# Kernel optimization log

Hardware: AMD Instinct MI355X
Metric: run time of the kernel (lower is better)

## Reference

```python
import jax, jax.numpy as jnp
import numpy as np

COUNTS = [1536, 8192, 16384, 24576, 12288, 1024, 512, 512, 256, 128, 128]
OFFS = np.concatenate([[0], np.cumsum(COUNTS)]).astype(int).tolist()
N = OFFS[-1]          # 65536 atoms total, sorted by degree
MAX_DEG = 10
BATCH = 2048          # fixed GraphGather batch size
F_IN = 75
GC = 256
DENSE = 512
N_TASKS = 12
N_CLASSES = 2
BN_EPS = 1e-3         # keras BatchNormalization default epsilon


def _graph_conv(x, deg_adjs, w0, wself, wneigh, b):
    # deepchem GraphConv: per-degree (self @ Wself + sum_neighbors @ Wneigh + b), relu
    outs = [x[OFFS[0]:OFFS[1]] @ w0 + b[0]]  # degree-0 atoms: self transform only
    for d in range(1, MAX_DEG + 1):
        self_atoms = x[OFFS[d]:OFFS[d + 1]]            # [n_d, F]
        neigh = x[deg_adjs[d - 1]].sum(axis=1)         # gather [n_d, d, F] -> sum -> [n_d, F]
        outs.append(self_atoms @ wself[d - 1] + neigh @ wneigh[d - 1] + b[d])
    return jax.nn.relu(jnp.concatenate(outs, axis=0))


def _graph_pool(x, deg_adjs):
    # deepchem GraphPool: elementwise max over {self} U neighbors, per degree
    outs = [x[OFFS[0]:OFFS[1]]]  # degree-0 atoms pass through
    for d in range(1, MAX_DEG + 1):
        self_atoms = x[OFFS[d]:OFFS[d + 1]]
        outs.append(jnp.maximum(self_atoms, x[deg_adjs[d - 1]].max(axis=1)))
    return jnp.concatenate(outs, axis=0)


def _bn(x, g, bta, m, v):
    # inference-mode BatchNormalization (training=False -> moving stats)
    return g * (x - m) * jax.lax.rsqrt(v + BN_EPS) + bta


def setup_inputs():
    key = jax.random.key(0)
    ks = iter(jax.random.split(key, 64))
    inp = {}
    inp["atom_features"] = jax.random.normal(next(ks), (N, F_IN), jnp.float32)
    inp["degree_slice"] = jnp.asarray(
        np.stack([np.array(OFFS[:-1]), np.array(COUNTS)], axis=1), jnp.int32)
    # each molecule gets exactly N/BATCH atoms so no GraphGather segment is empty
    inp["membership"] = jax.random.permutation(
        next(ks), jnp.arange(N, dtype=jnp.int32) % BATCH)
    inp["n_samples"] = BATCH
    for d in range(1, MAX_DEG + 1):
        inp["deg_adj_%d" % d] = jax.random.randint(
            next(ks), (COUNTS[d], d), 0, N, jnp.int32)

    def lin(k, fi, fo):
        return jax.random.normal(k, (fi, fo), jnp.float32) * np.float32(1.0 / np.sqrt(fi))

    for li, fi in [(1, F_IN), (2, GC)]:
        inp["gc%d_w0" % li] = lin(next(ks), fi, GC)
        inp["gc%d_wself" % li] = jnp.stack([lin(next(ks), fi, GC) for _ in range(MAX_DEG)])
        inp["gc%d_wneigh" % li] = jnp.stack([lin(next(ks), fi, GC) for _ in range(MAX_DEG)])
        inp["gc%d_b" % li] = jnp.zeros((MAX_DEG + 1, GC), jnp.float32)
    for bi, dim in [(1, GC), (2, GC), (3, DENSE)]:
        inp["bn%d_gamma" % bi] = jnp.ones((dim,), jnp.float32)
        inp["bn%d_beta" % bi] = jnp.zeros((dim,), jnp.float32)
        inp["bn%d_mean" % bi] = jnp.zeros((dim,), jnp.float32)
        inp["bn%d_var" % bi] = jnp.ones((dim,), jnp.float32)
    inp["dense_w"] = lin(next(ks), GC, DENSE)
    inp["dense_b"] = jnp.zeros((DENSE,), jnp.float32)
    inp["out_w"] = lin(next(ks), 2 * DENSE, N_TASKS * N_CLASSES)
    inp["out_b"] = jnp.zeros((N_TASKS * N_CLASSES,), jnp.float32)
    return inp


def reference(atom_features, degree_slice, membership, n_samples,
              deg_adj_1, deg_adj_2, deg_adj_3, deg_adj_4, deg_adj_5,
              deg_adj_6, deg_adj_7, deg_adj_8, deg_adj_9, deg_adj_10,
              gc1_w0, gc1_wself, gc1_wneigh, gc1_b,
              gc2_w0, gc2_wself, gc2_wneigh, gc2_b,
              bn1_gamma, bn1_beta, bn1_mean, bn1_var,
              bn2_gamma, bn2_beta, bn2_mean, bn2_var,
              bn3_gamma, bn3_beta, bn3_mean, bn3_var,
              dense_w, dense_b, out_w, out_b):
    deg_adjs = [deg_adj_1, deg_adj_2, deg_adj_3, deg_adj_4, deg_adj_5,
                deg_adj_6, deg_adj_7, deg_adj_8, deg_adj_9, deg_adj_10]
    h = _graph_conv(atom_features, deg_adjs, gc1_w0, gc1_wself, gc1_wneigh, gc1_b)
    h = _bn(h, bn1_gamma, bn1_beta, bn1_mean, bn1_var)
    h = _graph_pool(h, deg_adjs)
    h = _graph_conv(h, deg_adjs, gc2_w0, gc2_wself, gc2_wneigh, gc2_b)
    h = _bn(h, bn2_gamma, bn2_beta, bn2_mean, bn2_var)
    h = _graph_pool(h, deg_adjs)
    h = jax.nn.relu(h @ dense_w + dense_b)
    h = _bn(h, bn3_gamma, bn3_beta, bn3_mean, bn3_var)
    # GraphGather: tanh(concat(segment_sum, segment_max))
    ssum = jax.ops.segment_sum(h, membership, num_segments=BATCH)
    smax = jax.ops.segment_max(h, membership, num_segments=BATCH)
    fp = jnp.tanh(jnp.concatenate([ssum, smax], axis=1))   # [BATCH, 2*DENSE]
    logits = (fp @ out_w + out_b).reshape(BATCH, N_TASKS, N_CLASSES)[:n_samples]
    probs = jax.nn.softmax(logits, axis=-1)
    return probs, logits, fp
```

## Files before the change

### kernel.cpp

```cpp
#include <hip/hip_runtime.h>
#include <hip/hip_fp16.h>
#include <math.h>

#define NATOMS 65536

typedef _Float16 f16_t;
typedef __attribute__((ext_vector_type(8))) _Float16 half8;
typedef __attribute__((ext_vector_type(4))) float f32x4;

__constant__ int c_offs[12] = {0,1536,9728,26112,50688,62976,64000,64512,65024,65280,65408,65536};

struct Adj { const int* p[10]; };

__device__ __forceinline__ int seg_of(int row) {
    int s = 0;
#pragma unroll
    for (int i = 1; i <= 10; ++i) s += (row >= c_offs[i]) ? 1 : 0;
    return s;
}

__device__ __forceinline__ void glds16(const f16_t* g, f16_t* l) {
    __builtin_amdgcn_global_load_lds(
        (const __attribute__((address_space(1))) unsigned int*)g,
        (__attribute__((address_space(3))) unsigned int*)l,
        16, 0, 0);
}


__global__ void pack_w1(const float* __restrict__ w0, const float* __restrict__ wself,
                        const float* __restrict__ wneigh, f16_t* __restrict__ Wp) {
    int idx = blockIdx.x * 256 + threadIdx.x;
    int j = idx & 7, lane = (idx >> 3) & 63;
    int kb = (idx >> 9) % 6;
    int rest = idx / (512 * 6);
    int ni = rest & 15, s = rest >> 4;
    int k = kb * 32 + (lane >> 4) * 8 + j;
    int n = ni * 16 + (lane & 15);
    float v = 0.f;
    if (k < 75) v = (s == 0) ? w0[k*256 + n] : wself[((s-1)*75 + k)*256 + n];
    else if (k >= 96 && k < 171 && s > 0) v = wneigh[((s-1)*75 + (k-96))*256 + n];
    Wp[idx] = (f16_t)v;
}

__global__ void pack_w2(const float* __restrict__ w0, const float* __restrict__ wself,
                        const float* __restrict__ wneigh, f16_t* __restrict__ Wp) {
    int idx = blockIdx.x * 256 + threadIdx.x;
    int j = idx & 7, lane = (idx >> 3) & 63;
    int kb = (idx >> 9) & 15;
    int rest = idx >> 13;
    int ni = rest & 15, s = rest >> 4;
    int k = kb * 32 + (lane >> 4) * 8 + j;
    int n = ni * 16 + (lane & 15);
    float v = 0.f;
    if (k < 256) v = (s == 0) ? w0[k*256 + n] : wself[((s-1)*256 + k)*256 + n];
    else if (s > 0) v = wneigh[((s-1)*256 + (k-256))*256 + n];
    Wp[idx] = (f16_t)v;
}

__global__ void pack_wd(const float* __restrict__ w, f16_t* __restrict__ Wp) {
    int idx = blockIdx.x * 256 + threadIdx.x;
    int j = idx & 7, lane = (idx >> 3) & 63;
    int kb = (idx >> 9) & 7;
    int ni = (idx >> 12) & 31;
    int k = kb * 32 + (lane >> 4) * 8 + j;
    int n = ni * 16 + (lane & 15);
    Wp[idx] = (f16_t)w[(size_t)k*512 + n];
}

__global__ void cvt_pad(const float* __restrict__ xf, f16_t* __restrict__ xq) {
    int idx = blockIdx.x * 256 + threadIdx.x;
    int r = idx / 96;
    int c = idx - r * 96;
    xq[idx] = (c < 75) ? (f16_t)xf[(size_t)r*75 + c] : (f16_t)0.f;
}

template<int D, bool ISMAX, int LD>
__device__ __forceinline__ void gathD(float* v, const f16_t* __restrict__ src,
                                      const int* __restrict__ ap, int c) {
    int rows[D];
#pragma unroll
    for (int j = 0; j < D; ++j) rows[j] = ap[j];
    uint4 raw[D];
#pragma unroll
    for (int j = 0; j < D; ++j) raw[j] = *(const uint4*)(src + (size_t)rows[j]*LD + c);
#pragma unroll
    for (int j = 0; j < D; ++j) {
        const f16_t* u = (const f16_t*)&raw[j];
#pragma unroll
        for (int e = 0; e < 8; ++e) {
            float f = (float)u[e];
            v[e] = ISMAX ? fmaxf(v[e], f) : (v[e] + f);
        }
    }
}

template<bool ISMAX, int LD>
__device__ __forceinline__ void gath_switch(float* v, const f16_t* __restrict__ src,
                                            const int* __restrict__ ap, int s, int c) {
    switch (s) {
        case 1:  gathD<1,ISMAX,LD>(v,src,ap,c);  break;
        case 2:  gathD<2,ISMAX,LD>(v,src,ap,c);  break;
        case 3:  gathD<3,ISMAX,LD>(v,src,ap,c);  break;
        case 4:  gathD<4,ISMAX,LD>(v,src,ap,c);  break;
        case 5:  gathD<5,ISMAX,LD>(v,src,ap,c);  break;
        case 6:  gathD<6,ISMAX,LD>(v,src,ap,c);  break;
        case 7:  gathD<7,ISMAX,LD>(v,src,ap,c);  break;
        case 8:  gathD<8,ISMAX,LD>(v,src,ap,c);  break;
        case 9:  gathD<9,ISMAX,LD>(v,src,ap,c);  break;
        case 10: gathD<10,ISMAX,LD>(v,src,ap,c); break;
        default: break;
    }
}

__global__ __launch_bounds__(256) void nbsum_x(const f16_t* __restrict__ xq, f16_t* __restrict__ NBX, Adj adj) {
    int idx = blockIdx.x * 256 + threadIdx.x;
    int r = idx >> 4;
    int cc = idx & 15;
    if (cc >= 12) return;
    int c = cc << 3;
    int s = seg_of(r);
    float v[8];
#pragma unroll
    for (int e = 0; e < 8; ++e) v[e] = 0.f;
    if (s > 0)
        gath_switch<false,96>(v, xq, adj.p[s-1] + (size_t)(r - c_offs[s]) * s, s, c);
    f16_t o[8];
#pragma unroll
    for (int e = 0; e < 8; ++e) o[e] = (f16_t)v[e];
    *(uint4*)(NBX + (size_t)r*96 + c) = *(uint4*)o;
}

__global__ __launch_bounds__(256) void pool_k(const f16_t* __restrict__ H, f16_t* __restrict__ P, Adj adj) {
    int idx = blockIdx.x * 256 + threadIdx.x;
    int r = idx >> 5;
    int c = (idx & 31) << 3;
    int s = seg_of(r);
    uint4 self = *(const uint4*)(H + (size_t)r*256 + c);
    const f16_t* hp = (const f16_t*)&self;
    float v[8];
#pragma unroll
    for (int e = 0; e < 8; ++e) v[e] = (float)hp[e];
    if (s > 0)
        gath_switch<true,256>(v, H, adj.p[s-1] + (size_t)(r - c_offs[s]) * s, s, c);
    f16_t o[8];
#pragma unroll
    for (int e = 0; e < 8; ++e) o[e] = (f16_t)v[e];
    *(uint4*)(P + (size_t)r*256 + c) = *(uint4*)o;
}

__global__ __launch_bounds__(256) void nbsum_k(const f16_t* __restrict__ P, f16_t* __restrict__ NB, Adj adj) {
    int idx = blockIdx.x * 256 + threadIdx.x;
    int r = idx >> 5;
    int c = (idx & 31) << 3;
    int s = seg_of(r);
    float v[8];
#pragma unroll
    for (int e = 0; e < 8; ++e) v[e] = 0.f;
    if (s > 0)
        gath_switch<false,256>(v, P, adj.p[s-1] + (size_t)(r - c_offs[s]) * s, s, c);
    f16_t o[8];
#pragma unroll
    for (int e = 0; e < 8; ++e) o[e] = (f16_t)v[e];
    *(uint4*)(NB + (size_t)r*256 + c) = *(uint4*)o;
}

template<int K, int KSPLIT, int LDA, int N, int NY, bool SEG>
__global__ __launch_bounds__(256)
void gemm_mfma(const f16_t* __restrict__ A0, const f16_t* __restrict__ A1,
               const f16_t* __restrict__ Wp,
               const float* __restrict__ bias,
               const float* __restrict__ bng, const float* __restrict__ bnb,
               const float* __restrict__ bnm, const float* __restrict__ bnv,
               f16_t* __restrict__ C)
{
    constexpr int NKB = K / 32;
    constexpr int NNT = N / 16;
    __shared__ char smem[17408];
    f16_t* sA = (f16_t*)smem;
    f16_t* sB = sA + 4096;
    f16_t* eps = (f16_t*)smem;

    const int t = threadIdx.x;
    const int lane = t & 63, wave = t >> 6;
    const int wm = wave >> 1, wn = wave & 1;
    const int quad = lane >> 4, l16 = lane & 15;
    const int id = blockIdx.x;
    const int xcd = id & 7;
    const int jj = id >> 3;
    const int xi = jj / NY;
    const int y  = jj - xi * NY;
    const int r0 = (xi * 8 + xcd) * 128;
    const int n0 = y * 128;
    const int seg = SEG ? seg_of(r0) : 0;
    const int nbase = n0 >> 4;

    f32x4 acc[4][4];
#pragma unroll
    for (int mi = 0; mi < 4; ++mi)
#pragma unroll
        for (int ni = 0; ni < 4; ++ni) acc[mi][ni] = (f32x4){0.f,0.f,0.f,0.f};

    size_t aoff[2];
#pragma unroll
    for (int i = 0; i < 2; ++i)
        aoff[i] = (size_t)(r0 + (wave*2 + i)*16 + l16) * LDA + quad*8;
    size_t bbase[2];
#pragma unroll
    for (int i = 0; i < 2; ++i)
        bbase[i] = ((size_t)(seg*NNT + nbase + wave*2 + i) * NKB) * 512 + lane*8;

#pragma unroll
    for (int kb = 0; kb < NKB; ++kb) {
        const int kg = kb * 32;
        const f16_t* Ab = (kg < KSPLIT) ? (A0 + kg) : (A1 + (kg - KSPLIT));
#pragma unroll
        for (int i = 0; i < 2; ++i) {
            glds16(Ab + aoff[i], sA + (wave*2 + i)*512);
            glds16(Wp + bbase[i] + (size_t)kb*512, sB + (wave*2 + i)*512);
        }
        __syncthreads();
        half8 a[4], b[4];
#pragma unroll
        for (int mi = 0; mi < 4; ++mi)
            a[mi] = *(const half8*)(sA + (wm*4 + mi)*512 + lane*8);
#pragma unroll
        for (int ni = 0; ni < 4; ++ni)
            b[ni] = *(const half8*)(sB + (wn*4 + ni)*512 + lane*8);
#pragma unroll
        for (int mi = 0; mi < 4; ++mi)
#pragma unroll
            for (int ni = 0; ni < 4; ++ni)
                acc[mi][ni] = __builtin_amdgcn_mfma_f32_16x16x32_f16(a[mi], b[ni], acc[mi][ni], 0, 0, 0);
        __syncthreads();
    }

#pragma unroll
    for (int p = 0; p < 2; ++p) {
        if (wm == p) {
#pragma unroll
            for (int ni = 0; ni < 4; ++ni) {
                const int lcol = (wn*4 + ni)*16 + l16;
                const int col = n0 + lcol;
                const float scale = bng[col] * rsqrtf(bnv[col] + 1e-3f);
                const float shift = bnb[col] - bnm[col] * scale;
                const float bv = bias[(SEG ? seg*N : 0) + col];
#pragma unroll
                for (int mi = 0; mi < 4; ++mi) {
                    const int lrowb = mi*16 + quad*4;
#pragma unroll
                    for (int r = 0; r < 4; ++r) {
                        float v = acc[mi][ni][r] + bv;
                        v = fmaxf(v, 0.f);
                        v = fmaf(v, scale, shift);
                        eps[(lrowb + r)*136 + lcol] = (f16_t)v;
                    }
                }
            }
        }
        __syncthreads();
#pragma unroll
        for (int it = 0; it < 4; ++it) {
            int row = it*16 + (t >> 4);
            int ch  = t & 15;
            uint4 v = *(const uint4*)&eps[row*136 + ch*8];
            *(uint4*)(C + (size_t)(r0 + p*64 + row)*N + n0 + ch*8) = v;
        }
        __syncthreads();
    }
}

__global__ void scatter_k(const int* __restrict__ mem, int* __restrict__ counts, int* __restrict__ slots) {
    int i = blockIdx.x * 256 + threadIdx.x;
    int s = mem[i];
    int p = atomicAdd(&counts[s], 1);
    if (p < 32) slots[s*32 + p] = i;
}

__global__ __launch_bounds__(256)
void reduce_k(const f16_t* __restrict__ H3, const int* __restrict__ slots, float* __restrict__ fp) {
    int s = blockIdx.x, t = threadIdx.x;
    const int* sl = slots + s*32;
    float s0 = 0.f, s1 = 0.f, m0 = -INFINITY, m1 = -INFINITY;
#pragma unroll
    for (int i = 0; i < 32; i += 4) {
        int a[4];
#pragma unroll
        for (int j = 0; j < 4; ++j) a[j] = sl[i+j];
        float v0[4], v1[4];
#pragma unroll
        for (int j = 0; j < 4; ++j) {
            const f16_t* hr = H3 + (size_t)a[j]*512;
            v0[j] = (float)hr[t]; v1[j] = (float)hr[t+256];
        }
#pragma unroll
        for (int j = 0; j < 4; ++j) {
            s0 += v0[j]; s1 += v1[j];
            m0 = fmaxf(m0, v0[j]); m1 = fmaxf(m1, v1[j]);
        }
    }
    float* fr = fp + (size_t)s*1024;
    fr[t]       = tanhf(s0);
    fr[t+256]   = tanhf(s1);
    fr[512+t]   = tanhf(m0);
    fr[768+t]   = tanhf(m1);
}

__global__ __launch_bounds__(256)
void final_k(const float* __restrict__ fp, const float* __restrict__ out_w,
             const float* __restrict__ out_b, float* __restrict__ probs, float* __restrict__ logits) {
    __shared__ float row[1024];
    __shared__ float lg[24];
    int s = blockIdx.x, t = threadIdx.x;
    const float* fr = fp + (size_t)s*1024;
    *(float4*)&row[t*4] = *(const float4*)&fr[t*4];
    __syncthreads();
    if (t < 192) {
        int o = t >> 3;
        int k0 = (t & 7) * 128;
        float acc = 0.f;
        for (int k = 0; k < 128; ++k)
            acc = fmaf(row[k0+k], out_w[(size_t)(k0+k)*24 + o], acc);
        acc += __shfl_xor(acc, 1);
        acc += __shfl_xor(acc, 2);
        acc += __shfl_xor(acc, 4);
        if ((t & 7) == 0) lg[o] = acc + out_b[o];
    }
    __syncthreads();
    if (t < 12) {
        float l0 = lg[2*t], l1 = lg[2*t+1];
        float m = fmaxf(l0, l1);
        float e0 = expf(l0-m), e1 = expf(l1-m);
        float inv = 1.f / (e0 + e1);
        int base = s*24 + 2*t;
        probs[base]   = e0*inv;  probs[base+1]  = e1*inv;
        logits[base]  = l0;      logits[base+1] = l1;
    }
}

extern "C" void kernel_launch(void* const* d_in, const int* in_sizes, int n_in,
                              void* d_out, int out_size, void* d_ws, size_t ws_size,
                              hipStream_t stream) {
    const float* atom       = (const float*)d_in[0];
    const int*   membership = (const int*)  d_in[2];
    Adj adj;
    for (int d = 0; d < 10; ++d) adj.p[d] = (const int*)d_in[4+d];
    const float* gc1_w0     = (const float*)d_in[14];
    const float* gc1_wself  = (const float*)d_in[15];
    const float* gc1_wneigh = (const float*)d_in[16];
    const float* gc1_b      = (const float*)d_in[17];
    const float* gc2_w0     = (const float*)d_in[18];
    const float* gc2_wself  = (const float*)d_in[19];
    const float* gc2_wneigh = (const float*)d_in[20];
    const float* gc2_b      = (const float*)d_in[21];
    const float* bn1g = (const float*)d_in[22]; const float* bn1b = (const float*)d_in[23];
    const float* bn1m = (const float*)d_in[24]; const float* bn1v = (const float*)d_in[25];
    const float* bn2g = (const float*)d_in[26]; const float* bn2b = (const float*)d_in[27];
    const float* bn2m = (const float*)d_in[28]; const float* bn2v = (const float*)d_in[29];
    const float* bn3g = (const float*)d_in[30]; const float* bn3b = (const float*)d_in[31];
    const float* bn3m = (const float*)d_in[32]; const float* bn3v = (const float*)d_in[33];
    const float* dense_w = (const float*)d_in[34];
    const float* dense_b = (const float*)d_in[35];
    const float* out_w   = (const float*)d_in[36];
    const float* out_b   = (const float*)d_in[37];

    f16_t* wsb = (f16_t*)d_ws;
    f16_t* xq   = wsb;
    f16_t* NBX  = wsb + 6291456;
    f16_t* H1b  = wsb + 12582912;
    f16_t* P1b  = wsb + 29360128;
    f16_t* NB2b = wsb + 46137344;
    f16_t* H2b  = H1b;
    f16_t* P2b  = NB2b;
    f16_t* H3b  = H1b;
    f16_t* W1p  = wsb + 62914560;
    f16_t* W2p  = wsb + 63455232;
    f16_t* Wdp  = wsb + 64897024;
    int*  counts = (int*)(wsb + 65028096);
    int*  slots  = counts + 2048;

    float* outp   = (float*)d_out;
    float* probs  = outp;
    float* logits = outp + 49152;
    float* fp     = outp + 98304;

    pack_w1<<<2112, 256, 0, stream>>>(gc1_w0, gc1_wself, gc1_wneigh, W1p);
    pack_w2<<<5632, 256, 0, stream>>>(gc2_w0, gc2_wself, gc2_wneigh, W2p);
    pack_wd<<<512,  256, 0, stream>>>(dense_w, Wdp);

    cvt_pad<<<(NATOMS*96)/256, 256, 0, stream>>>(atom, xq);
    nbsum_x<<<(NATOMS*16)/256, 256, 0, stream>>>(xq, NBX, adj);
    gemm_mfma<192,96,96,256,2,true><<<1024, 256, 0, stream>>>(
        xq, NBX, W1p, gc1_b, bn1g, bn1b, bn1m, bn1v, H1b);
    pool_k<<<(NATOMS*32)/256, 256, 0, stream>>>(H1b, P1b, adj);

    nbsum_k<<<(NATOMS*32)/256, 256, 0, stream>>>(P1b, NB2b, adj);
    gemm_mfma<512,256,256,256,2,true><<<1024, 256, 0, stream>>>(
        P1b, NB2b, W2p, gc2_b, bn2g, bn2b, bn2m, bn2v, H2b);
    pool_k<<<(NATOMS*32)/256, 256, 0, stream>>>(H2b, P2b, adj);

    gemm_mfma<256,256,256,512,4,false><<<2048, 256, 0, stream>>>(
        P2b, P2b, Wdp, dense_b, bn3g, bn3b, bn3m, bn3v, H3b);

    hipMemsetAsync((void*)counts, 0, 2048*sizeof(int), stream);
    scatter_k<<<NATOMS/256, 256, 0, stream>>>(membership, counts, slots);
    reduce_k<<<2048, 256, 0, stream>>>(H3b, slots, fp);

    final_k<<<2048, 256, 0, stream>>>(fp, out_w, out_b, probs, logits);
}
```

Baseline: 391.0 us.

## Compute output logits with MFMA GEMM and vectorize GraphGather reduction

The per-sample scalar output layer (one block per sample, with strided fp32 weight reads) is replaced by a batched f16 MFMA GEMM over all 2048 fingerprints against a packed, zero-padded output weight. Softmax is fused into the GEMM epilogue using a lane shuffle. The segment reduction now uses 64-thread blocks with 16-byte vector loads, and also writes an f16 copy of the fingerprint to feed the GEMM. This adds a weight-pack kernel, and the logits are computed from f16-rounded fingerprints, which lowers their precision.

```diff
diff --git a/kernel.cpp b/kernel.cpp
--- a/kernel.cpp
+++ b/kernel.cpp
@@ -65,6 +65,16 @@
     int k = kb * 32 + (lane >> 4) * 8 + j;
     int n = ni * 16 + (lane & 15);
     Wp[idx] = (f16_t)w[(size_t)k*512 + n];
+}
+
+__global__ void pack_wo(const float* __restrict__ w, f16_t* __restrict__ Wp) {
+    int idx = blockIdx.x * 256 + threadIdx.x;
+    int j = idx & 7, lane = (idx >> 3) & 63;
+    int kb = (idx >> 9) & 31;
+    int ni = idx >> 14;
+    int k = kb * 32 + (lane >> 4) * 8 + j;
+    int n = ni * 16 + (lane & 15);
+    Wp[idx] = (n < 24) ? (f16_t)w[k*24 + n] : (f16_t)0.f;
 }
 
 __global__ void cvt_pad(const float* __restrict__ xf, f16_t* __restrict__ xq) {
@@ -276,64 +286,116 @@
     if (p < 32) slots[s*32 + p] = i;
 }
 
+__global__ __launch_bounds__(64)
+void reduce_k(const f16_t* __restrict__ H3, const int* __restrict__ slots,
+              float* __restrict__ fp, f16_t* __restrict__ fph) {
+    int s = blockIdx.x, l = threadIdx.x;
+    int c = l * 8;
+    const int* sl = slots + s*32;
+    float sm[8], mx[8];
+#pragma unroll
+    for (int e = 0; e < 8; ++e) { sm[e] = 0.f; mx[e] = -INFINITY; }
+#pragma unroll
+    for (int i = 0; i < 32; ++i) {
+        int a = sl[i];
+        uint4 raw = *(const uint4*)(H3 + (size_t)a*512 + c);
+        const f16_t* u = (const f16_t*)&raw;
+#pragma unroll
+        for (int e = 0; e < 8; ++e) {
+            float f = (float)u[e];
+            sm[e] += f;
+            mx[e] = fmaxf(mx[e], f);
+        }
+    }
+    float o1[8], o2[8];
+    f16_t h1[8], h2[8];
+#pragma unroll
+    for (int e = 0; e < 8; ++e) {
+        o1[e] = tanhf(sm[e]); o2[e] = tanhf(mx[e]);
+        h1[e] = (f16_t)o1[e]; h2[e] = (f16_t)o2[e];
+    }
+    float* fr = fp + (size_t)s*1024;
+    *(float4*)(fr + c)       = *(float4*)&o1[0];
+    *(float4*)(fr + c + 4)   = *(float4*)&o1[4];
+    *(float4*)(fr + 512 + c)     = *(float4*)&o2[0];
+    *(float4*)(fr + 512 + c + 4) = *(float4*)&o2[4];
+    f16_t* fh = fph + (size_t)s*1024;
+    *(uint4*)(fh + c)       = *(uint4*)h1;
+    *(uint4*)(fh + 512 + c) = *(uint4*)h2;
+}
+
 __global__ __launch_bounds__(256)
-void reduce_k(const f16_t* __restrict__ H3, const int* __restrict__ slots, float* __restrict__ fp) {
-    int s = blockIdx.x, t = threadIdx.x;
-    const int* sl = slots + s*32;
-    float s0 = 0.f, s1 = 0.f, m0 = -INFINITY, m1 = -INFINITY;
-#pragma unroll
-    for (int i = 0; i < 32; i += 4) {
-        int a[4];
-#pragma unroll
-        for (int j = 0; j < 4; ++j) a[j] = sl[i+j];
-        float v0[4], v1[4];
-#pragma unroll
-        for (int j = 0; j < 4; ++j) {
-            const f16_t* hr = H3 + (size_t)a[j]*512;
-            v0[j] = (float)hr[t]; v1[j] = (float)hr[t+256];
-        }
-#pragma unroll
-        for (int j = 0; j < 4; ++j) {
-            s0 += v0[j]; s1 += v1[j];
-            m0 = fmaxf(m0, v0[j]); m1 = fmaxf(m1, v1[j]);
-        }
-    }
-    float* fr = fp + (size_t)s*1024;
-    fr[t]       = tanhf(s0);
-    fr[t+256]   = tanhf(s1);
-    fr[512+t]   = tanhf(m0);
-    fr[768+t]   = tanhf(m1);
-}
-
-__global__ __launch_bounds__(256)
-void final_k(const float* __restrict__ fp, const float* __restrict__ out_w,
-             const float* __restrict__ out_b, float* __restrict__ probs, float* __restrict__ logits) {
-    __shared__ float row[1024];
-    __shared__ float lg[24];
-    int s = blockIdx.x, t = threadIdx.x;
-    const float* fr = fp + (size_t)s*1024;
-    *(float4*)&row[t*4] = *(const float4*)&fr[t*4];
-    __syncthreads();
-    if (t < 192) {
-        int o = t >> 3;
-        int k0 = (t & 7) * 128;
-        float acc = 0.f;
-        for (int k = 0; k < 128; ++k)
-            acc = fmaf(row[k0+k], out_w[(size_t)(k0+k)*24 + o], acc);
-        acc += __shfl_xor(acc, 1);
-        acc += __shfl_xor(acc, 2);
-        acc += __shfl_xor(acc, 4);
-        if ((t & 7) == 0) lg[o] = acc + out_b[o];
-    }
-    __syncthreads();
-    if (t < 12) {
-        float l0 = lg[2*t], l1 = lg[2*t+1];
-        float m = fmaxf(l0, l1);
-        float e0 = expf(l0-m), e1 = expf(l1-m);
-        float inv = 1.f / (e0 + e1);
-        int base = s*24 + 2*t;
-        probs[base]   = e0*inv;  probs[base+1]  = e1*inv;
-        logits[base]  = l0;      logits[base+1] = l1;
+void final_mfma(const f16_t* __restrict__ fph, const f16_t* __restrict__ Wop,
+                const float* __restrict__ out_b,
+                float* __restrict__ probs, float* __restrict__ logits) {
+    const int t = threadIdx.x;
+    const int lane = t & 63, wave = t >> 6;
+    const int quad = lane >> 4, l16 = lane & 15;
+    const int r0 = blockIdx.x * 256 + wave * 64;
+
+    f32x4 acc[4][2];
+#pragma unroll
+    for (int mi = 0; mi < 4; ++mi)
+#pragma unroll
+        for (int ni = 0; ni < 2; ++ni) acc[mi][ni] = (f32x4){0.f,0.f,0.f,0.f};
+
+    size_t rowoff[4];
+#pragma unroll
+    for (int mi = 0; mi < 4; ++mi)
+        rowoff[mi] = (size_t)(r0 + mi*16 + l16) * 1024 + quad*8;
+    size_t boff[2];
+#pragma unroll
+    for (int ni = 0; ni < 2; ++ni)
+        boff[ni] = (size_t)ni * 32 * 512 + lane*8;
+
+    auto loadA = [&](half8* a, int kb) {
+#pragma unroll
+        for (int mi = 0; mi < 4; ++mi) a[mi] = *(const half8*)(fph + rowoff[mi] + kb*32);
+    };
+    auto loadB = [&](half8* b, int kb) {
+#pragma unroll
+        for (int ni = 0; ni < 2; ++ni) b[ni] = *(const half8*)(Wop + boff[ni] + (size_t)kb*512);
+    };
+    auto domfma = [&](half8* a, half8* b) {
+#pragma unroll
+        for (int mi = 0; mi < 4; ++mi)
+#pragma unroll
+            for (int ni = 0; ni < 2; ++ni)
+                acc[mi][ni] = __builtin_amdgcn_mfma_f32_16x16x32_f16(a[mi], b[ni], acc[mi][ni], 0, 0, 0);
+    };
+
+    half8 a0[4], b0[2], a1[4], b1[2];
+    loadA(a0, 0); loadB(b0, 0);
+#pragma unroll
+    for (int kb = 0; kb < 32; kb += 2) {
+        loadA(a1, kb + 1); loadB(b1, kb + 1);
+        domfma(a0, b0);
+        if (kb + 2 < 32) { loadA(a0, kb + 2); loadB(b0, kb + 2); }
+        domfma(a1, b1);
+    }
+
+#pragma unroll
+    for (int ni = 0; ni < 2; ++ni) {
+        const int c = ni*16 + l16;
+        const bool ok = (c < 24);
+        const float bv = ok ? out_b[c] : 0.f;
+#pragma unroll
+        for (int mi = 0; mi < 4; ++mi) {
+#pragma unroll
+            for (int r = 0; r < 4; ++r) {
+                float lg = acc[mi][ni][r] + bv;
+                float lp = __shfl_xor(lg, 1);
+                float m = fmaxf(lg, lp);
+                float e  = expf(lg - m);
+                float ep = expf(lp - m);
+                float pr = e / (e + ep);
+                if (ok) {
+                    int row = r0 + mi*16 + quad*4 + r;
+                    logits[(size_t)row*24 + c] = lg;
+                    probs[(size_t)row*24 + c]  = pr;
+                }
+            }
+        }
     }
 }
 
@@ -375,7 +437,9 @@
     f16_t* W1p  = wsb + 62914560;
     f16_t* W2p  = wsb + 63455232;
     f16_t* Wdp  = wsb + 64897024;
-    int*  counts = (int*)(wsb + 65028096);
+    f16_t* fph  = wsb + 65028096;
+    f16_t* Wop  = wsb + 67125248;
+    int*  counts = (int*)(wsb + 67158016);
     int*  slots  = counts + 2048;
 
     float* outp   = (float*)d_out;
@@ -386,6 +450,7 @@
     pack_w1<<<2112, 256, 0, stream>>>(gc1_w0, gc1_wself, gc1_wneigh, W1p);
     pack_w2<<<5632, 256, 0, stream>>>(gc2_w0, gc2_wself, gc2_wneigh, W2p);
     pack_wd<<<512,  256, 0, stream>>>(dense_w, Wdp);
+    pack_wo<<<128,  256, 0, stream>>>(out_w, Wop);
 
     cvt_pad<<<(NATOMS*96)/256, 256, 0, stream>>>(atom, xq);
     nbsum_x<<<(NATOMS*16)/256, 256, 0, stream>>>(xq, NBX, adj);
@@ -403,7 +468,7 @@
 
     hipMemsetAsync((void*)counts, 0, 2048*sizeof(int), stream);
     scatter_k<<<NATOMS/256, 256, 0, stream>>>(membership, counts, slots);
-    reduce_k<<<2048, 256, 0, stream>>>(H3b, slots, fp);
-
-    final_k<<<2048, 256, 0, stream>>>(fp, out_w, out_b, probs, logits);
-}
+    reduce_k<<<2048, 64, 0, stream>>>(H3b, slots, fp, fph);
+
+    final_mfma<<<8, 256, 0, stream>>>(fph, Wop, out_b, probs, logits);
+}
```

Measured after the change: 385.4 us. No clear change (-1.4%).
